# Optimization experiments

Hardware: AMD Instinct MI355X
Metric: run time of the kernel (lower is better)

## Reference

```python
import jax, jax.numpy as jnp
import numpy as np

B, C_IN, N = 8, 256, 4096
D_KQ, D_OUT = 64, 256


def setup_inputs() -> dict:
    key = jax.random.key(0)
    k1, k2, k3, k4 = jax.random.split(key, 4)
    x = jax.random.normal(k1, (B, C_IN, N), dtype=jnp.float32)
    # 1x1 Conv1d weights (out_ch, in_ch); kaiming-ish scale
    Wq = jax.random.normal(k2, (D_KQ, C_IN), dtype=jnp.float32) * (1.0 / np.sqrt(C_IN))
    Wk = jax.random.normal(k3, (D_KQ, C_IN), dtype=jnp.float32) * (1.0 / np.sqrt(C_IN))
    Wv = jax.random.normal(k4, (D_OUT, C_IN), dtype=jnp.float32) * (1.0 / np.sqrt(C_IN))
    return {"x": x, "Wq": Wq, "Wk": Wk, "Wv": Wv}


def reference(x, Wq, Wk, Wv):
    # 1x1 conv projections == channel matmuls
    # q, k: (B, N, D_KQ) / (B, D_KQ, N); v: (B, N, D_OUT)
    temperature = jnp.asarray(Wq.shape[0], x.dtype) ** 0.5
    q = jnp.einsum('bcn,kc->bnk', x, Wq)  # (B, N, d_kq)
    k = jnp.einsum('bcn,kc->bkn', x, Wk)  # (B, d_kq, N)
    v = jnp.einsum('bcn,oc->bno', x, Wv)  # (B, N, d_out)
    attn = jnp.einsum('bnk,bkm->bnm', q / temperature, k)  # (B, N, N)
    attn = jax.nn.softmax(attn, axis=-1)  # dropout is identity in eval
    y = jnp.einsum('bnm,bmo->bno', attn, v)  # (B, N, d_out)
    return jnp.transpose(y, (0, 2, 1))  # (B, d_out, N)
```

## Files before the change

kernel.cpp:

```cpp
#include <hip/hip_runtime.h>
#include <hip/hip_bf16.h>

#define NB   8
#define CIN  256
#define NN   4096
#define DK   64
#define DOUT 256
#define NT   (NN / 64)
#define VTILE_BYTES (DOUT * 64 * 2)
#define JTOT 384

typedef float f32x4 __attribute__((ext_vector_type(4)));
typedef short short8 __attribute__((ext_vector_type(8)));
typedef short short4s __attribute__((ext_vector_type(4)));

__device__ __forceinline__ short f2bf(float f) {
    unsigned u = __builtin_bit_cast(unsigned, f);
    u = (u + 0x7FFFu + ((u >> 16) & 1u)) >> 16;
    return (short)u;
}

__device__ __forceinline__ int vtile_byte(int o, int j) {
    return o * 128 + ((((j >> 3) ^ (o & 7)) << 4)) + ((j & 7) << 1);
}

__device__ __forceinline__ void gload_lds16(const void* g, void* l) {
    __builtin_amdgcn_global_load_lds(
        (const __attribute__((address_space(1))) void*)g,
        (__attribute__((address_space(3))) void*)l, 16, 0, 0);
}

__global__ __launch_bounds__(256) void convw_kernel(
    const float* __restrict__ Wq, const float* __restrict__ Wk,
    const float* __restrict__ Wv, short* __restrict__ Wb)
{
    const int j = blockIdx.x;
    const int c = threadIdx.x;
    float v;
    if (j < 64)       v = Wq[j * CIN + c] * 0.18033688011f;
    else if (j < 128) v = Wk[(j - 64) * CIN + c];
    else              v = Wv[(j - 128) * CIN + c];
    Wb[(size_t)j * CIN + c] = f2bf(v);
}

__global__ __launch_bounds__(256) void proj_kernel(
    const float* __restrict__ x, const short* __restrict__ Wb,
    short* __restrict__ Qw, short* __restrict__ Kw, short* __restrict__ Vw)
{
    __shared__ short Xt[64][256];
    const int t  = threadIdx.x;
    const int nt = blockIdx.x;
    const int b  = blockIdx.y;
    const int n0 = nt * 64;
    const int w  = t >> 6;
    const int l  = t & 63;
    const int hi = l >> 4, lo = l & 15;

    {
        const float* xs = x + (size_t)b * CIN * NN + (size_t)(w * 64) * NN + n0 + l;
        #pragma unroll
        for (int c8 = 0; c8 < 8; ++c8) {
            short8 v;
            #pragma unroll
            for (int i = 0; i < 8; ++i)
                v[i] = f2bf(xs[(size_t)(c8 * 8 + i) * NN]);
            const int c0 = w * 64 + c8 * 8;
            *(short8*)((char*)&Xt[0][0] + l * 512 + ((((c0 >> 3) ^ (l & 7)) << 4)))
                = v;
        }
    }
    __syncthreads();

    const int wj0 = w * 96;
    f32x4 acc[6][4];
    #pragma unroll
    for (int jt = 0; jt < 6; ++jt)
        #pragma unroll
        for (int ntl = 0; ntl < 4; ++ntl) acc[jt][ntl] = f32x4{0.f, 0.f, 0.f, 0.f};

    #pragma unroll 2
    for (int kb = 0; kb < 8; ++kb) {
        short8 aw[6], bx[4];
        #pragma unroll
        for (int jt = 0; jt < 6; ++jt)
            aw[jt] = *(const short8*)(Wb + (size_t)(wj0 + jt * 16 + lo) * CIN
                                         + kb * 32 + hi * 8);
        #pragma unroll
        for (int ntl = 0; ntl < 4; ++ntl) {
            const int n = ntl * 16 + lo;
            bx[ntl] = *(const short8*)((char*)&Xt[0][0] + n * 512
                                       + ((((kb * 4 + hi) ^ (n & 7)) << 4)));
        }
        #pragma unroll
        for (int jt = 0; jt < 6; ++jt)
            #pragma unroll
            for (int ntl = 0; ntl < 4; ++ntl)
                acc[jt][ntl] = __builtin_amdgcn_mfma_f32_16x16x32_bf16(
                    aw[jt], bx[ntl], acc[jt][ntl], 0, 0, 0);
    }

    #pragma unroll
    for (int jt = 0; jt < 6; ++jt) {
        const int jbase = wj0 + jt * 16;
        #pragma unroll
        for (int ntl = 0; ntl < 4; ++ntl) {
            const f32x4 a = acc[jt][ntl];
            const int n = ntl * 16 + lo;
            if (jbase < 64) {
                short4s pk;
                #pragma unroll
                for (int r = 0; r < 4; ++r) pk[r] = f2bf(a[r]);
                *(short4s*)(Qw + (size_t)b * NN * DK + (size_t)(n0 + n) * DK
                            + jbase + hi * 4) = pk;
            } else if (jbase < 128) {
                short4s pk;
                #pragma unroll
                for (int r = 0; r < 4; ++r) pk[r] = f2bf(a[r]);
                *(short4s*)(Kw + (size_t)b * NN * DK + (size_t)(n0 + n) * DK
                            + (jbase - 64) + hi * 4) = pk;
            } else {
                const int o0 = jbase - 128 + hi * 4;
                char* vtile = (char*)(Vw + (size_t)b * DOUT * NN)
                            + (size_t)nt * VTILE_BYTES;
                #pragma unroll
                for (int r = 0; r < 4; ++r)
                    *(short*)(vtile + vtile_byte(o0 + r, n)) = f2bf(a[r]);
            }
        }
    }
}

__global__ __launch_bounds__(256) void attn_kernel(
    const short* __restrict__ Q, const short* __restrict__ K,
    const short* __restrict__ Vt, float* __restrict__ out)
{
    __shared__ short Vlds[2][DOUT * 64];
    __shared__ short P_lds[4][16][72];
    const int b  = blockIdx.y;
    const int q0 = blockIdx.x * 64;
    const int w  = threadIdx.x >> 6;
    const int l  = threadIdx.x & 63;
    const int hi = l >> 4, lo = l & 15;

    const short* Qb = Q  + (size_t)b * NN * DK;
    const short* Kb = K  + (size_t)b * NN * DK;
    const char*  Vbase = (const char*)(Vt + (size_t)b * DOUT * NN);

    const int qrow = q0 + w * 16 + lo;
    const short8 aq0 = *(const short8*)(Qb + (size_t)qrow * DK + hi * 8);
    const short8 aq1 = *(const short8*)(Qb + (size_t)qrow * DK + hi * 8 + 32);

    const int lo7 = lo & 7;
    const int sw0 = ((hi ^ lo7) << 4);
    const int sw1 = (((4 + hi) ^ lo7) << 4);

    f32x4 oacc[16];
    #pragma unroll
    for (int i = 0; i < 16; ++i) oacc[i] = f32x4{0.f, 0.f, 0.f, 0.f};
    float mrun[4], lrun[4];
    #pragma unroll
    for (int r = 0; r < 4; ++r) { mrun[r] = -1e30f; lrun[r] = 0.f; }

    {
        const char* vtile = Vbase;
        #pragma unroll
        for (int kk = 0; kk < 8; ++kk) {
            const int c = kk * 4 + w;
            gload_lds16(vtile + c * 1024 + l * 16,
                        (char*)&Vlds[0][0] + c * 1024);
        }
    }
    asm volatile("s_waitcnt vmcnt(0)" ::: "memory");
    __builtin_amdgcn_s_barrier();
    __builtin_amdgcn_sched_barrier(0);

    for (int t = 0; t < NT; ++t) {
        const int cur = t & 1;
        const int m0  = t * 64;

        short8 bk0[4], bk1[4];
        #pragma unroll
        for (int mt = 0; mt < 4; ++mt) {
            const short* kr = Kb + (size_t)(m0 + mt * 16 + lo) * DK + hi * 8;
            bk0[mt] = *(const short8*)(kr);
            bk1[mt] = *(const short8*)(kr + 32);
        }
        __builtin_amdgcn_sched_barrier(0);

        {
            const int tn = (t + 1 < NT) ? t + 1 : NT - 1;
            const char* vtile = Vbase + (size_t)tn * VTILE_BYTES;
            #pragma unroll
            for (int kk = 0; kk < 8; ++kk) {
                const int c = kk * 4 + w;
                gload_lds16(vtile + c * 1024 + l * 16,
                            (char*)&Vlds[cur ^ 1][0] + c * 1024);
            }
        }
        __builtin_amdgcn_sched_barrier(0);

        f32x4 s[4];
        #pragma unroll
        for (int mt = 0; mt < 4; ++mt) {
            f32x4 acc = {0.f, 0.f, 0.f, 0.f};
            acc = __builtin_amdgcn_mfma_f32_16x16x32_bf16(aq0, bk0[mt], acc, 0, 0, 0);
            acc = __builtin_amdgcn_mfma_f32_16x16x32_bf16(aq1, bk1[mt], acc, 0, 0, 0);
            s[mt] = acc;
        }
        float rmax[4], rsum[4], alpha[4];
        #pragma unroll
        for (int r = 0; r < 4; ++r)
            rmax[r] = fmaxf(fmaxf(s[0][r], s[1][r]), fmaxf(s[2][r], s[3][r]));
        #pragma unroll
        for (int d = 1; d < 16; d <<= 1) {
            #pragma unroll
            for (int r = 0; r < 4; ++r)
                rmax[r] = fmaxf(rmax[r], __shfl_xor(rmax[r], d, 64));
        }
        #pragma unroll
        for (int r = 0; r < 4; ++r) {
            float mn = fmaxf(mrun[r], rmax[r]);
            alpha[r] = __builtin_amdgcn_exp2f(mrun[r] - mn);
            mrun[r] = mn;
            rsum[r] = 0.f;
        }
        #pragma unroll
        for (int mt = 0; mt < 4; ++mt) {
            #pragma unroll
            for (int r = 0; r < 4; ++r) {
                float p = __builtin_amdgcn_exp2f(s[mt][r] - mrun[r]);
                s[mt][r] = p;
                rsum[r] += p;
            }
        }
        #pragma unroll
        for (int d = 1; d < 16; d <<= 1) {
            #pragma unroll
            for (int r = 0; r < 4; ++r)
                rsum[r] += __shfl_xor(rsum[r], d, 64);
        }
        bool resc = false;
        #pragma unroll
        for (int r = 0; r < 4; ++r) {
            lrun[r] = lrun[r] * alpha[r] + rsum[r];
            resc |= (alpha[r] != 1.f);
        }
        if (__any(resc)) {
            #pragma unroll
            for (int i = 0; i < 16; ++i) {
                #pragma unroll
                for (int r = 0; r < 4; ++r) oacc[i][r] *= alpha[r];
            }
        }
        #pragma unroll
        for (int mt = 0; mt < 4; ++mt) {
            #pragma unroll
            for (int r = 0; r < 4; ++r)
                P_lds[w][hi * 4 + r][mt * 16 + lo] = f2bf(s[mt][r]);
        }
        asm volatile("s_waitcnt lgkmcnt(0)" ::: "memory");
        __builtin_amdgcn_sched_barrier(0);
        short8 pa0 = *(const short8*)(&P_lds[w][lo][hi * 8]);
        short8 pa1 = *(const short8*)(&P_lds[w][lo][hi * 8 + 32]);

        const char* vb = (const char*)&Vlds[cur][0];
        #pragma unroll
        for (int ot = 0; ot < 16; ++ot) {
            const char* rowp = vb + (ot * 16 + lo) * 128;
            short8 bv0 = *(const short8*)(rowp + sw0);
            short8 bv1 = *(const short8*)(rowp + sw1);
            oacc[ot] = __builtin_amdgcn_mfma_f32_16x16x32_bf16(pa0, bv0, oacc[ot], 0, 0, 0);
            oacc[ot] = __builtin_amdgcn_mfma_f32_16x16x32_bf16(pa1, bv1, oacc[ot], 0, 0, 0);
        }

        __builtin_amdgcn_sched_barrier(0);
        asm volatile("s_waitcnt vmcnt(0)" ::: "memory");
        __builtin_amdgcn_s_barrier();
        __builtin_amdgcn_sched_barrier(0);
    }
    float inv[4];
    #pragma unroll
    for (int r = 0; r < 4; ++r) inv[r] = 1.f / lrun[r];
    float* ob = out + (size_t)b * DOUT * NN;
    #pragma unroll
    for (int ot = 0; ot < 16; ++ot) {
        #pragma unroll
        for (int r = 0; r < 4; ++r)
            ob[(size_t)(ot * 16 + lo) * NN + (q0 + w * 16 + hi * 4 + r)]
                = oacc[ot][r] * inv[r];
    }
}

extern "C" void kernel_launch(void* const* d_in, const int* in_sizes, int n_in,
                              void* d_out, int out_size, void* d_ws, size_t ws_size,
                              hipStream_t stream)
{
    const float* x  = (const float*)d_in[0];
    const float* Wq = (const float*)d_in[1];
    const float* Wk = (const float*)d_in[2];
    const float* Wv = (const float*)d_in[3];
    float* out = (float*)d_out;

    short* Qw = (short*)d_ws;
    short* Kw = Qw + (size_t)NB * NN * DK;
    short* Vw = Kw + (size_t)NB * NN * DK;
    short* Wb = (short*)d_out;

    convw_kernel<<<dim3(JTOT), 256, 0, stream>>>(Wq, Wk, Wv, Wb);
    proj_kernel<<<dim3(NN / 64, NB), 256, 0, stream>>>(x, Wb, Qw, Kw, Vw);
    attn_kernel<<<dim3(NN / 64, NB), 256, 0, stream>>>(Qw, Kw, Vw, out);
}
```

Before: 308.7 us.

## Use lazy softmax max rescaling, deferred row sums, and packed bf16 conversions

The attention loop now rescales the running max only when a tile's local max exceeds the stored max by a threshold of 8 (in log2 units). This skips the max shuffle-reduction and the output rescale on most tiles. The row sum is kept per lane and reduced across lanes once at the end, which removes a per-tile shuffle reduction. Probabilities and the projection outputs are packed to bf16 with v_cvt_pk_bf16_f32, and P is stored in a key-permuted order that matches a permuted V tile layout written by the projection kernel, so both use wider stores. The risk is exponentials up to 2^8 before renormalization, which bf16 P can hold, and a correctness dependence on the P and V permutations matching.

```diff
diff --git a/kernel.cpp b/kernel.cpp
--- a/kernel.cpp
+++ b/kernel.cpp
@@ -13,15 +13,22 @@
 typedef float f32x4 __attribute__((ext_vector_type(4)));
 typedef short short8 __attribute__((ext_vector_type(8)));
 typedef short short4s __attribute__((ext_vector_type(4)));
+typedef int   int2v  __attribute__((ext_vector_type(2)));
+typedef int   int4v  __attribute__((ext_vector_type(4)));
 
 __device__ __forceinline__ short f2bf(float f) {
     unsigned u = __builtin_bit_cast(unsigned, f);
     u = (u + 0x7FFFu + ((u >> 16) & 1u)) >> 16;
     return (short)u;
 }
-
-__device__ __forceinline__ int vtile_byte(int o, int j) {
-    return o * 128 + ((((j >> 3) ^ (o & 7)) << 4)) + ((j & 7) << 1);
+__device__ __forceinline__ int pkbf(float a, float b) {
+    int r;
+    asm("v_cvt_pk_bf16_f32 %0, %1, %2" : "=v"(r) : "v"(a), "v"(b));
+    return r;
+}
+
+__device__ __forceinline__ int vtile_byte(int o, int c) {
+    return o * 128 + ((((c >> 3) ^ (o & 7)) << 4)) + ((c & 7) << 1);
 }
 
 __device__ __forceinline__ void gload_lds16(const void* g, void* l) {
@@ -60,13 +67,16 @@
         const float* xs = x + (size_t)b * CIN * NN + (size_t)(w * 64) * NN + n0 + l;
         #pragma unroll
         for (int c8 = 0; c8 < 8; ++c8) {
-            short8 v;
+            float f[8];
             #pragma unroll
             for (int i = 0; i < 8; ++i)
-                v[i] = f2bf(xs[(size_t)(c8 * 8 + i) * NN]);
+                f[i] = xs[(size_t)(c8 * 8 + i) * NN];
+            int4v pk;
+            #pragma unroll
+            for (int j = 0; j < 4; ++j) pk[j] = pkbf(f[2 * j], f[2 * j + 1]);
             const int c0 = w * 64 + c8 * 8;
-            *(short8*)((char*)&Xt[0][0] + l * 512 + ((((c0 >> 3) ^ (l & 7)) << 4)))
-                = v;
+            *(int4v*)((char*)&Xt[0][0] + l * 512 + ((((c0 >> 3) ^ (l & 7)) << 4)))
+                = pk;
         }
     }
     __syncthreads();
@@ -102,29 +112,30 @@
     #pragma unroll
     for (int jt = 0; jt < 6; ++jt) {
         const int jbase = wj0 + jt * 16;
-        #pragma unroll
-        for (int ntl = 0; ntl < 4; ++ntl) {
-            const f32x4 a = acc[jt][ntl];
-            const int n = ntl * 16 + lo;
-            if (jbase < 64) {
+        if (jbase < 128) {
+            #pragma unroll
+            for (int ntl = 0; ntl < 4; ++ntl) {
+                const f32x4 a = acc[jt][ntl];
+                const int n = ntl * 16 + lo;
                 short4s pk;
                 #pragma unroll
                 for (int r = 0; r < 4; ++r) pk[r] = f2bf(a[r]);
-                *(short4s*)(Qw + (size_t)b * NN * DK + (size_t)(n0 + n) * DK
-                            + jbase + hi * 4) = pk;
-            } else if (jbase < 128) {
-                short4s pk;
-                #pragma unroll
-                for (int r = 0; r < 4; ++r) pk[r] = f2bf(a[r]);
-                *(short4s*)(Kw + (size_t)b * NN * DK + (size_t)(n0 + n) * DK
-                            + (jbase - 64) + hi * 4) = pk;
-            } else {
-                const int o0 = jbase - 128 + hi * 4;
-                char* vtile = (char*)(Vw + (size_t)b * DOUT * NN)
-                            + (size_t)nt * VTILE_BYTES;
-                #pragma unroll
-                for (int r = 0; r < 4; ++r)
-                    *(short*)(vtile + vtile_byte(o0 + r, n)) = f2bf(a[r]);
+                short* base = (jbase < 64)
+                    ? (Qw + (size_t)b * NN * DK + (size_t)(n0 + n) * DK + jbase)
+                    : (Kw + (size_t)b * NN * DK + (size_t)(n0 + n) * DK + (jbase - 64));
+                *(short4s*)(base + hi * 4) = pk;
+            }
+        } else {
+            char* vtile = (char*)(Vw + (size_t)b * DOUT * NN)
+                        + (size_t)nt * VTILE_BYTES;
+            #pragma unroll
+            for (int r = 0; r < 4; ++r) {
+                const int o = jbase - 128 + hi * 4 + r;
+                int2v pk;
+                pk[0] = pkbf(acc[jt][0][r], acc[jt][1][r]);
+                pk[1] = pkbf(acc[jt][2][r], acc[jt][3][r]);
+                *(int2v*)(vtile + o * 128 + ((((lo >> 1) ^ (o & 7)) << 4))
+                          + ((lo & 1) << 3)) = pk;
             }
         }
     }
@@ -157,9 +168,9 @@
     f32x4 oacc[16];
     #pragma unroll
     for (int i = 0; i < 16; ++i) oacc[i] = f32x4{0.f, 0.f, 0.f, 0.f};
-    float mrun[4], lrun[4];
-    #pragma unroll
-    for (int r = 0; r < 4; ++r) { mrun[r] = -1e30f; lrun[r] = 0.f; }
+    float mrun[4], mthr[4], lpart[4];
+    #pragma unroll
+    for (int r = 0; r < 4; ++r) { mrun[r] = -1e30f; mthr[r] = -1e29f; lpart[r] = 0.f; }
 
     {
         const char* vtile = Vbase;
@@ -207,45 +218,32 @@
             acc = __builtin_amdgcn_mfma_f32_16x16x32_bf16(aq1, bk1[mt], acc, 0, 0, 0);
             s[mt] = acc;
         }
-        float rmax[4], rsum[4], alpha[4];
+
+        float lmax[4];
         #pragma unroll
         for (int r = 0; r < 4; ++r)
-            rmax[r] = fmaxf(fmaxf(s[0][r], s[1][r]), fmaxf(s[2][r], s[3][r]));
-        #pragma unroll
-        for (int d = 1; d < 16; d <<= 1) {
-            #pragma unroll
-            for (int r = 0; r < 4; ++r)
-                rmax[r] = fmaxf(rmax[r], __shfl_xor(rmax[r], d, 64));
-        }
-        #pragma unroll
-        for (int r = 0; r < 4; ++r) {
-            float mn = fmaxf(mrun[r], rmax[r]);
-            alpha[r] = __builtin_amdgcn_exp2f(mrun[r] - mn);
-            mrun[r] = mn;
-            rsum[r] = 0.f;
-        }
-        #pragma unroll
-        for (int mt = 0; mt < 4; ++mt) {
+            lmax[r] = fmaxf(fmaxf(s[0][r], s[1][r]), fmaxf(s[2][r], s[3][r]));
+        bool need = false;
+        #pragma unroll
+        for (int r = 0; r < 4; ++r) need |= (lmax[r] > mthr[r]);
+        if (__any(need)) {
+            float rmax[4], alpha[4];
+            #pragma unroll
+            for (int r = 0; r < 4; ++r) rmax[r] = lmax[r];
+            #pragma unroll
+            for (int d = 1; d < 16; d <<= 1) {
+                #pragma unroll
+                for (int r = 0; r < 4; ++r)
+                    rmax[r] = fmaxf(rmax[r], __shfl_xor(rmax[r], d, 64));
+            }
             #pragma unroll
             for (int r = 0; r < 4; ++r) {
-                float p = __builtin_amdgcn_exp2f(s[mt][r] - mrun[r]);
-                s[mt][r] = p;
-                rsum[r] += p;
-            }
-        }
-        #pragma unroll
-        for (int d = 1; d < 16; d <<= 1) {
-            #pragma unroll
-            for (int r = 0; r < 4; ++r)
-                rsum[r] += __shfl_xor(rsum[r], d, 64);
-        }
-        bool resc = false;
-        #pragma unroll
-        for (int r = 0; r < 4; ++r) {
-            lrun[r] = lrun[r] * alpha[r] + rsum[r];
-            resc |= (alpha[r] != 1.f);
-        }
-        if (__any(resc)) {
+                float mn = fmaxf(mrun[r], rmax[r]);
+                alpha[r] = __builtin_amdgcn_exp2f(mrun[r] - mn);
+                mrun[r] = mn;
+                mthr[r] = mn + 8.f;
+                lpart[r] *= alpha[r];
+            }
             #pragma unroll
             for (int i = 0; i < 16; ++i) {
                 #pragma unroll
@@ -256,7 +254,18 @@
         for (int mt = 0; mt < 4; ++mt) {
             #pragma unroll
             for (int r = 0; r < 4; ++r)
-                P_lds[w][hi * 4 + r][mt * 16 + lo] = f2bf(s[mt][r]);
+                s[mt][r] = __builtin_amdgcn_exp2f(s[mt][r] - mrun[r]);
+        }
+        #pragma unroll
+        for (int r = 0; r < 4; ++r)
+            lpart[r] += (s[0][r] + s[1][r]) + (s[2][r] + s[3][r]);
+
+        #pragma unroll
+        for (int r = 0; r < 4; ++r) {
+            int2v pk;
+            pk[0] = pkbf(s[0][r], s[1][r]);
+            pk[1] = pkbf(s[2][r], s[3][r]);
+            *(int2v*)(&P_lds[w][hi * 4 + r][lo * 4]) = pk;
         }
         asm volatile("s_waitcnt lgkmcnt(0)" ::: "memory");
         __builtin_amdgcn_sched_barrier(0);
@@ -278,9 +287,15 @@
         __builtin_amdgcn_s_barrier();
         __builtin_amdgcn_sched_barrier(0);
     }
+    #pragma unroll
+    for (int d = 1; d < 16; d <<= 1) {
+        #pragma unroll
+        for (int r = 0; r < 4; ++r)
+            lpart[r] += __shfl_xor(lpart[r], d, 64);
+    }
     float inv[4];
     #pragma unroll
-    for (int r = 0; r < 4; ++r) inv[r] = 1.f / lrun[r];
+    for (int r = 0; r < 4; ++r) inv[r] = 1.f / lpart[r];
     float* ob = out + (size_t)b * DOUT * NN;
     #pragma unroll
     for (int ot = 0; ot < 16; ++ot) {
```

Result: slower. 418.2 us (+35.5%).
